# Kernel optimization log

Hardware: AMD Instinct MI355X
Metric: run time of the kernel (lower is better)

## Reference

```python
import jax, jax.numpy as jnp
import numpy as np

B, L, D = 64, 512, 768

def setup_inputs() -> dict:
    key = jax.random.key(0)
    k1, k2, k3, k4 = jax.random.split(key, 4)
    hidden_states = jax.random.normal(k1, (B, L, D), dtype=jnp.float32)
    # nn.Linear(hidden_size, hidden_size): weight [D, D], bias [D]
    W = jax.random.normal(k2, (D, D), dtype=jnp.float32) * (1.0 / np.sqrt(D))
    b = jax.random.normal(k3, (D,), dtype=jnp.float32) * 0.02
    # context_vector: [D, 1]
    context_vector = jax.random.normal(k4, (D, 1), dtype=jnp.float32)
    return {"hidden_states": hidden_states, "W": W, "b": b, "context_vector": context_vector}

def reference(hidden_states, W, b, context_vector):
    # tanh(dense(h)): [B, L, D]; torch Linear uses x @ W.T + b
    proj = jnp.tanh(jnp.einsum('bld,ed->ble', hidden_states, W) + b)
    # scores: [B, L]
    scores = jnp.einsum('bld,d->bl', proj, context_vector[:, 0])
    # softmax over sequence dim (dim=1)
    attention_weights = jax.nn.softmax(scores, axis=1)
    # weighted sum over sequence: [B, D]
    weighted_output = jnp.einsum('bld,bl->bd', hidden_states, attention_weights)
    return (weighted_output, attention_weights)
```

## Files before the change

kernel.cpp:

```cpp
#include <hip/hip_runtime.h>
#include <hip/hip_bf16.h>


using half8 = __attribute__((ext_vector_type(8))) _Float16;
using f32x4 = __attribute__((ext_vector_type(4))) float;

#define AS1 __attribute__((address_space(1)))
#define AS3 __attribute__((address_space(3)))

__device__ __forceinline__ void gload_lds16(const void* g, void* l) {
  __builtin_amdgcn_global_load_lds((const AS1 void*)g, (AS3 void*)l, 16, 0, 0);
}

__device__ __forceinline__ unsigned short f2h(float x) {
  _Float16 h = (_Float16)x;
  return __builtin_bit_cast(unsigned short, h);
}

__device__ __forceinline__ float tanh_fast(float x) {
  return 1.0f - __fdividef(2.0f, 1.0f + __expf(2.0f * x));
}


__global__ void convert_h(const float4* __restrict__ H4, ushort4* __restrict__ Ah) {
  int i = blockIdx.x * 256 + threadIdx.x;
  float4 x = H4[i];
  ushort4 o;
  o.x = f2h(x.x); o.y = f2h(x.y); o.z = f2h(x.z); o.w = f2h(x.w);
  Ah[i] = o;
}

__global__ void convert_w(const float4* __restrict__ W4, ushort4* __restrict__ Wt) {
  int i = blockIdx.x * 256 + threadIdx.x;
  float4 x = W4[i];
  ushort4 o;
  o.x = f2h(x.x); o.y = f2h(x.y); o.z = f2h(x.z); o.w = f2h(x.w);
  Wt[i] = o;
}


__device__ __forceinline__ void stage_tiles32(const char* abase, const char* bbase,
                                              char* ldsAbuf, char* ldsBbuf, int tid) {
  char* ldsAw = ldsAbuf + ((tid >> 6) << 10);
  char* ldsBw = ldsBbuf + ((tid >> 6) << 10);
  #pragma unroll
  for (int r = 0; r < 2; ++r) {
    int off = tid * 16 + r * 4096;
    int row = off >> 6;
    int col = (off & 63) ^ ((row & 3) << 4);
    gload_lds16(abase + row * 1536 + col, ldsAw + r * 4096);
  }
  #pragma unroll
  for (int r = 0; r < 2; ++r) {
    int off = tid * 16 + r * 4096;
    int row = off >> 6;
    int col = (off & 63) ^ ((row & 3) << 4);
    gload_lds16(bbase + row * 1536 + col, ldsBw + r * 4096);
  }
}

__device__ __forceinline__ void compute_tile32(const ushort* ldsAbuf, const ushort* ldsBbuf,
                                               int wr, int wc, int m, int q,
                                               f32x4 acc[4][4]) {
  half8 areg[4], breg[4];
  #pragma unroll
  for (int mi = 0; mi < 4; ++mi) {
    int row = wr * 64 + mi * 16 + m;
    int col = (q * 16) ^ ((row & 3) << 4);
    areg[mi] = *(const half8*)((const char*)ldsAbuf + row * 64 + col);
  }
  #pragma unroll
  for (int ni = 0; ni < 4; ++ni) {
    int row = wc * 64 + ni * 16 + m;
    int col = (q * 16) ^ ((row & 3) << 4);
    breg[ni] = *(const half8*)((const char*)ldsBbuf + row * 64 + col);
  }
  #pragma unroll
  for (int mi = 0; mi < 4; ++mi)
    #pragma unroll
    for (int ni = 0; ni < 4; ++ni)
      acc[mi][ni] = __builtin_amdgcn_mfma_f32_16x16x32_f16(
          areg[mi], breg[ni], acc[mi][ni], 0, 0, 0);
}

__global__ __launch_bounds__(256, 4) void gemm_scores(
    const ushort* __restrict__ Ah, const ushort* __restrict__ Wt,
    const float* __restrict__ bias, const float* __restrict__ cvec,
    float* __restrict__ part) {
  __shared__ ushort ldsA[2][4096];
  __shared__ ushort ldsB[2][4096];
  __shared__ float scpart[2][128];

  const int tid = threadIdx.x;
  const int lane = tid & 63;
  const int wid = tid >> 6;
  const int wr = wid >> 1, wc = wid & 1;
  const int m = lane & 15, q = lane >> 4;

  const int bid = blockIdx.x;
  const int xcd = bid & 7;
  const int slot = bid >> 3;
  const int mtile = xcd * 32 + slot / 6;
  const int ntile = slot % 6;

  f32x4 acc[4][4];
  #pragma unroll
  for (int a = 0; a < 4; ++a)
    #pragma unroll
    for (int b2 = 0; b2 < 4; ++b2)
      acc[a][b2] = (f32x4){0.f, 0.f, 0.f, 0.f};

  const char* const abase0 = (const char*)Ah + (size_t)(mtile * 128) * 1536;
  const char* const bbase0 = (const char*)Wt + (size_t)(ntile * 128) * 1536;

  stage_tiles32(abase0, bbase0, (char*)ldsA[0], (char*)ldsB[0], tid);
  __syncthreads();

  #pragma unroll
  for (int kb2 = 0; kb2 < 12; ++kb2) {
    stage_tiles32(abase0 + (kb2 * 2 + 1) * 64, bbase0 + (kb2 * 2 + 1) * 64,
                  (char*)ldsA[1], (char*)ldsB[1], tid);
    compute_tile32(ldsA[0], ldsB[0], wr, wc, m, q, acc);
    __syncthreads();

    if (kb2 < 11)
      stage_tiles32(abase0 + (kb2 * 2 + 2) * 64, bbase0 + (kb2 * 2 + 2) * 64,
                    (char*)ldsA[0], (char*)ldsB[0], tid);
    compute_tile32(ldsA[1], ldsB[1], wr, wc, m, q, acc);
    __syncthreads();
  }

  float bb[4], cc[4];
  #pragma unroll
  for (int ni = 0; ni < 4; ++ni) {
    int e = ntile * 128 + wc * 64 + ni * 16 + m;
    bb[ni] = bias[e];
    cc[ni] = cvec[e];
  }
  #pragma unroll
  for (int mi = 0; mi < 4; ++mi) {
    #pragma unroll
    for (int j = 0; j < 4; ++j) {
      float s = 0.f;
      #pragma unroll
      for (int ni = 0; ni < 4; ++ni)
        s += tanh_fast(acc[mi][ni][j] + bb[ni]) * cc[ni];
      s += __shfl_xor(s, 1);
      s += __shfl_xor(s, 2);
      s += __shfl_xor(s, 4);
      s += __shfl_xor(s, 8);
      if (m == 0) scpart[wc][wr * 64 + mi * 16 + q * 4 + j] = s;
    }
  }
  __syncthreads();
  if (tid < 128)
    part[ntile * 32768 + mtile * 128 + tid] = scpart[0][tid] + scpart[1][tid];
}

__global__ void wsum_fused(const ushort* __restrict__ Ah, const float* __restrict__ prt,
                           float* __restrict__ out) {
  int b = blockIdx.x, dc = blockIdx.y;
  int t = threadIdx.x;
  __shared__ float w[512];
  __shared__ float redm[2], reds[2];

  float s[4];
  #pragma unroll
  for (int i = 0; i < 4; ++i) {
    int r = b * 512 + t + i * 128;
    s[i] = prt[r] + prt[32768 + r] + prt[2 * 32768 + r] +
           prt[3 * 32768 + r] + prt[4 * 32768 + r] + prt[5 * 32768 + r];
  }
  float mx = fmaxf(fmaxf(s[0], s[1]), fmaxf(s[2], s[3]));
  #pragma unroll
  for (int o = 32; o >= 1; o >>= 1) mx = fmaxf(mx, __shfl_xor(mx, o));
  if ((t & 63) == 0) redm[t >> 6] = mx;
  __syncthreads();
  mx = fmaxf(redm[0], redm[1]);

  float e[4], sm = 0.f;
  #pragma unroll
  for (int i = 0; i < 4; ++i) { e[i] = __expf(s[i] - mx); sm += e[i]; }
  #pragma unroll
  for (int o = 32; o >= 1; o >>= 1) sm += __shfl_xor(sm, o);
  if ((t & 63) == 0) reds[t >> 6] = sm;
  __syncthreads();
  float inv = 1.0f / (reds[0] + reds[1]);
  #pragma unroll
  for (int i = 0; i < 4; ++i) w[t + i * 128] = e[i] * inv;
  __syncthreads();

  int d0 = dc * 256 + t * 2;
  const ushort* hp = Ah + (size_t)b * 512 * 768 + d0;
  float a0 = 0.f, a1 = 0.f;
  #pragma unroll 8
  for (int l = 0; l < 512; ++l) {
    unsigned u = *(const unsigned*)(hp + (size_t)l * 768);
    float wl = w[l];
    a0 += wl * (float)__builtin_bit_cast(_Float16, (unsigned short)(u & 0xffff));
    a1 += wl * (float)__builtin_bit_cast(_Float16, (unsigned short)(u >> 16));
  }
  out[b * 768 + d0] = a0;
  out[b * 768 + d0 + 1] = a1;

  if (dc == 0) {
    #pragma unroll
    for (int i = 0; i < 4; ++i)
      out[49152 + b * 512 + t + i * 128] = w[t + i * 128];
  }
}

extern "C" void kernel_launch(void* const* d_in, const int* in_sizes, int n_in,
                              void* d_out, int out_size, void* d_ws, size_t ws_size,
                              hipStream_t stream) {
  const float* H    = (const float*)d_in[0];
  const float* W    = (const float*)d_in[1];
  const float* bias = (const float*)d_in[2];
  const float* cvec = (const float*)d_in[3];
  float* out = (float*)d_out;

  char* ws = (char*)d_ws;
  ushort* Ah = (ushort*)(ws + 0);
  ushort* Wt = (ushort*)(ws + 50331648);
  float*  prt = (float*)(ws + 51511296);

  hipLaunchKernelGGL(convert_h, dim3(24576), dim3(256), 0, stream,
                     (const float4*)H, (ushort4*)Ah);
  hipLaunchKernelGGL(convert_w, dim3(576), dim3(256), 0, stream,
                     (const float4*)W, (ushort4*)Wt);
  hipLaunchKernelGGL(gemm_scores, dim3(1536), dim3(256), 0, stream,
                     Ah, Wt, bias, cvec, prt);
  hipLaunchKernelGGL(wsum_fused, dim3(64, 3), dim3(128), 0, stream,
                     Ah, prt, out);
}
```

Measured before the change: 117.0 us.

## Restructure score GEMM into 128x256 tiles with 3-stage K=64 pipeline

The score GEMM now uses 512-thread blocks computing 128x256 output tiles, halving the grid and the number of partial-score slices from six to three. It stages K=64 chunks through a triple-buffered LDS pipeline with explicit vmcnt waits, split prefetch issue, and s_setprio around the MFMA bursts. The goal is more reuse of A tiles, fewer barriers per K step, and deeper overlap of global loads with compute. In exchange it uses more LDS per block, so occupancy drops, and the hand-tuned waitcnt logic is fragile.

```diff
diff --git a/kernel.cpp b/kernel.cpp
--- a/kernel.cpp
+++ b/kernel.cpp
@@ -38,102 +38,122 @@
   Wt[i] = o;
 }
 
-
-__device__ __forceinline__ void stage_tiles32(const char* abase, const char* bbase,
-                                              char* ldsAbuf, char* ldsBbuf, int tid) {
-  char* ldsAw = ldsAbuf + ((tid >> 6) << 10);
-  char* ldsBw = ldsBbuf + ((tid >> 6) << 10);
-  #pragma unroll
-  for (int r = 0; r < 2; ++r) {
-    int off = tid * 16 + r * 4096;
-    int row = off >> 6;
-    int col = (off & 63) ^ ((row & 3) << 4);
-    gload_lds16(abase + row * 1536 + col, ldsAw + r * 4096);
-  }
-  #pragma unroll
-  for (int r = 0; r < 2; ++r) {
-    int off = tid * 16 + r * 4096;
-    int row = off >> 6;
-    int col = (off & 63) ^ ((row & 3) << 4);
-    gload_lds16(bbase + row * 1536 + col, ldsBw + r * 4096);
-  }
-}
-
-__device__ __forceinline__ void compute_tile32(const ushort* ldsAbuf, const ushort* ldsBbuf,
-                                               int wr, int wc, int m, int q,
-                                               f32x4 acc[4][4]) {
-  half8 areg[4], breg[4];
-  #pragma unroll
-  for (int mi = 0; mi < 4; ++mi) {
-    int row = wr * 64 + mi * 16 + m;
-    int col = (q * 16) ^ ((row & 3) << 4);
-    areg[mi] = *(const half8*)((const char*)ldsAbuf + row * 64 + col);
-  }
-  #pragma unroll
-  for (int ni = 0; ni < 4; ++ni) {
-    int row = wc * 64 + ni * 16 + m;
-    int col = (q * 16) ^ ((row & 3) << 4);
-    breg[ni] = *(const half8*)((const char*)ldsBbuf + row * 64 + col);
-  }
-  #pragma unroll
-  for (int mi = 0; mi < 4; ++mi)
-    #pragma unroll
-    for (int ni = 0; ni < 4; ++ni)
-      acc[mi][ni] = __builtin_amdgcn_mfma_f32_16x16x32_f16(
-          areg[mi], breg[ni], acc[mi][ni], 0, 0, 0);
-}
-
-__global__ __launch_bounds__(256, 4) void gemm_scores(
+__global__ __launch_bounds__(512) void gemm_scores(
     const ushort* __restrict__ Ah, const ushort* __restrict__ Wt,
     const float* __restrict__ bias, const float* __restrict__ cvec,
     float* __restrict__ part) {
-  __shared__ ushort ldsA[2][4096];
-  __shared__ ushort ldsB[2][4096];
-  __shared__ float scpart[2][128];
+  __shared__ ushort ldsA[3][128 * 64];
+  __shared__ ushort ldsB[3][256 * 64];
+  __shared__ float scpart[4][128];
 
   const int tid = threadIdx.x;
   const int lane = tid & 63;
   const int wid = tid >> 6;
-  const int wr = wid >> 1, wc = wid & 1;
+  const int wr = wid >> 2;
+  const int wc = wid & 3;
   const int m = lane & 15, q = lane >> 4;
 
   const int bid = blockIdx.x;
   const int xcd = bid & 7;
-  const int slot = bid >> 3;
-  const int mtile = xcd * 32 + slot / 6;
-  const int ntile = slot % 6;
+  const int sid = bid >> 3;
+  const int mtile = xcd * 32 + sid / 3;
+  const int ntile = sid % 3;
+
+  const char* const Abase = (const char*)Ah + (size_t)(mtile * 128) * 1536;
+  const char* const Bbase = (const char*)Wt + (size_t)(ntile * 256) * 1536;
+  const int wavebase = (tid >> 6) << 10;
 
   f32x4 acc[4][4];
   #pragma unroll
-  for (int a = 0; a < 4; ++a)
-    #pragma unroll
-    for (int b2 = 0; b2 < 4; ++b2)
-      acc[a][b2] = (f32x4){0.f, 0.f, 0.f, 0.f};
-
-  const char* const abase0 = (const char*)Ah + (size_t)(mtile * 128) * 1536;
-  const char* const bbase0 = (const char*)Wt + (size_t)(ntile * 128) * 1536;
-
-  stage_tiles32(abase0, bbase0, (char*)ldsA[0], (char*)ldsB[0], tid);
-  __syncthreads();
-
-  #pragma unroll
-  for (int kb2 = 0; kb2 < 12; ++kb2) {
-    stage_tiles32(abase0 + (kb2 * 2 + 1) * 64, bbase0 + (kb2 * 2 + 1) * 64,
-                  (char*)ldsA[1], (char*)ldsB[1], tid);
-    compute_tile32(ldsA[0], ldsB[0], wr, wc, m, q, acc);
-    __syncthreads();
-
-    if (kb2 < 11)
-      stage_tiles32(abase0 + (kb2 * 2 + 2) * 64, bbase0 + (kb2 * 2 + 2) * 64,
-                    (char*)ldsA[0], (char*)ldsB[0], tid);
-    compute_tile32(ldsA[1], ldsB[1], wr, wc, m, q, acc);
-    __syncthreads();
+  for (int i = 0; i < 4; ++i)
+    #pragma unroll
+    for (int j = 0; j < 4; ++j)
+      acc[i][j] = (f32x4){0.f, 0.f, 0.f, 0.f};
+
+  auto stageA = [&](int kt, char* dst) {
+    #pragma unroll
+    for (int c = 0; c < 2; ++c) {
+      int off = tid * 16 + c * 8192;
+      int row = off >> 7;
+      int col = (off & 127) ^ ((row & 7) << 4);
+      gload_lds16(Abase + (size_t)row * 1536 + kt * 128 + col,
+                  dst + c * 8192 + wavebase);
+    }
+  };
+  auto stageBq = [&](int kt, char* dst, int c) {
+    int off = tid * 16 + c * 8192;
+    int row = off >> 7;
+    int col = (off & 127) ^ ((row & 7) << 4);
+    gload_lds16(Bbase + (size_t)row * 1536 + kt * 128 + col,
+                dst + c * 8192 + wavebase);
+  };
+
+  stageA(0, (char*)ldsA[0]);
+  #pragma unroll
+  for (int c = 0; c < 4; ++c) stageBq(0, (char*)ldsB[0], c);
+  stageA(1, (char*)ldsA[1]);
+  #pragma unroll
+  for (int c = 0; c < 4; ++c) stageBq(1, (char*)ldsB[1], c);
+  asm volatile("s_waitcnt vmcnt(6)" ::: "memory");
+  __builtin_amdgcn_s_barrier();
+
+  #pragma unroll
+  for (int t = 0; t < 12; ++t) {
+    const char* As = (const char*)ldsA[t % 3];
+    const char* Bs = (const char*)ldsB[t % 3];
+    char* dA = (char*)ldsA[(t + 2) % 3];
+    char* dB = (char*)ldsB[(t + 2) % 3];
+    const int st = t + 2;
+    half8 breg[4][2];
+    #pragma unroll
+    for (int p = 0; p < 2; ++p) {
+      half8 areg[2][2];
+      #pragma unroll
+      for (int dmi = 0; dmi < 2; ++dmi) {
+        int row = wr * 64 + (p * 2 + dmi) * 16 + m;
+        #pragma unroll
+        for (int ks = 0; ks < 2; ++ks)
+          areg[dmi][ks] = *(const half8*)(As + row * 128 +
+                                          ((ks * 64 + q * 16) ^ ((m & 7) << 4)));
+      }
+      if (p == 0) {
+        #pragma unroll
+        for (int ni = 0; ni < 4; ++ni) {
+          int row = wc * 64 + ni * 16 + m;
+          #pragma unroll
+          for (int ks = 0; ks < 2; ++ks)
+            breg[ni][ks] = *(const half8*)(Bs + row * 128 +
+                                           ((ks * 64 + q * 16) ^ ((m & 7) << 4)));
+        }
+      }
+      if (st < 12) {
+        if (p == 0) { stageA(st, dA); stageBq(st, dB, 0); }
+        else        { stageBq(st, dB, 1); stageBq(st, dB, 2); stageBq(st, dB, 3); }
+      }
+      if (p == 1) {
+        if (t < 10)       asm volatile("s_waitcnt vmcnt(6)" ::: "memory");
+        else if (t == 10) asm volatile("s_waitcnt vmcnt(0)" ::: "memory");
+      }
+      __builtin_amdgcn_s_barrier();
+      asm volatile("s_waitcnt lgkmcnt(0)" ::: "memory");
+      __builtin_amdgcn_s_setprio(1);
+      #pragma unroll
+      for (int ks = 0; ks < 2; ++ks)
+        #pragma unroll
+        for (int dmi = 0; dmi < 2; ++dmi)
+          #pragma unroll
+          for (int ni = 0; ni < 4; ++ni)
+            acc[p * 2 + dmi][ni] = __builtin_amdgcn_mfma_f32_16x16x32_f16(
+                areg[dmi][ks], breg[ni][ks], acc[p * 2 + dmi][ni], 0, 0, 0);
+      __builtin_amdgcn_s_setprio(0);
+      __builtin_amdgcn_s_barrier();
+    }
   }
 
   float bb[4], cc[4];
   #pragma unroll
   for (int ni = 0; ni < 4; ++ni) {
-    int e = ntile * 128 + wc * 64 + ni * 16 + m;
+    int e = ntile * 256 + wc * 64 + ni * 16 + m;
     bb[ni] = bias[e];
     cc[ni] = cvec[e];
   }
@@ -154,7 +174,8 @@
   }
   __syncthreads();
   if (tid < 128)
-    part[ntile * 32768 + mtile * 128 + tid] = scpart[0][tid] + scpart[1][tid];
+    part[ntile * 32768 + mtile * 128 + tid] =
+        scpart[0][tid] + scpart[1][tid] + scpart[2][tid] + scpart[3][tid];
 }
 
 __global__ void wsum_fused(const ushort* __restrict__ Ah, const float* __restrict__ prt,
@@ -168,8 +189,7 @@
   #pragma unroll
   for (int i = 0; i < 4; ++i) {
     int r = b * 512 + t + i * 128;
-    s[i] = prt[r] + prt[32768 + r] + prt[2 * 32768 + r] +
-           prt[3 * 32768 + r] + prt[4 * 32768 + r] + prt[5 * 32768 + r];
+    s[i] = prt[r] + prt[32768 + r] + prt[2 * 32768 + r];
   }
   float mx = fmaxf(fmaxf(s[0], s[1]), fmaxf(s[2], s[3]));
   #pragma unroll
@@ -228,7 +248,7 @@
                      (const float4*)H, (ushort4*)Ah);
   hipLaunchKernelGGL(convert_w, dim3(576), dim3(256), 0, stream,
                      (const float4*)W, (ushort4*)Wt);
-  hipLaunchKernelGGL(gemm_scores, dim3(1536), dim3(256), 0, stream,
+  hipLaunchKernelGGL(gemm_scores, dim3(768), dim3(512), 0, stream,
                      Ah, Wt, bias, cvec, prt);
   hipLaunchKernelGGL(wsum_fused, dim3(64, 3), dim3(128), 0, stream,
                      Ah, prt, out);
```

Measured after the change: 111.9 us. 1.05x faster.

## Compute full N=768 per block in GEMM, removing partial score reduction

Applied to the files above, without the earlier changes.

The GEMM now gives each 512-thread block a 128-row M tile across all 768 output columns, with 8 waves each covering 64x192. This removes the six-way N split, the partial-score buffer, and the six-way sum in the softmax kernel, and each A tile is loaded only once. In exchange the block holds 192 accumulator floats per thread and about 100KB of LDS, and the grid shrinks to 256 blocks. That lowers occupancy and may underfill the GPU's 256 CUs if spills or load imbalance occur.

```diff
diff --git a/kernel.cpp b/kernel.cpp
--- a/kernel.cpp
+++ b/kernel.cpp
@@ -38,102 +38,81 @@
   Wt[i] = o;
 }
 
-
-__device__ __forceinline__ void stage_tiles32(const char* abase, const char* bbase,
-                                              char* ldsAbuf, char* ldsBbuf, int tid) {
-  char* ldsAw = ldsAbuf + ((tid >> 6) << 10);
-  char* ldsBw = ldsBbuf + ((tid >> 6) << 10);
-  #pragma unroll
-  for (int r = 0; r < 2; ++r) {
-    int off = tid * 16 + r * 4096;
-    int row = off >> 6;
-    int col = (off & 63) ^ ((row & 3) << 4);
-    gload_lds16(abase + row * 1536 + col, ldsAw + r * 4096);
-  }
-  #pragma unroll
-  for (int r = 0; r < 2; ++r) {
-    int off = tid * 16 + r * 4096;
-    int row = off >> 6;
-    int col = (off & 63) ^ ((row & 3) << 4);
-    gload_lds16(bbase + row * 1536 + col, ldsBw + r * 4096);
-  }
-}
-
-__device__ __forceinline__ void compute_tile32(const ushort* ldsAbuf, const ushort* ldsBbuf,
-                                               int wr, int wc, int m, int q,
-                                               f32x4 acc[4][4]) {
-  half8 areg[4], breg[4];
-  #pragma unroll
-  for (int mi = 0; mi < 4; ++mi) {
-    int row = wr * 64 + mi * 16 + m;
-    int col = (q * 16) ^ ((row & 3) << 4);
-    areg[mi] = *(const half8*)((const char*)ldsAbuf + row * 64 + col);
-  }
-  #pragma unroll
-  for (int ni = 0; ni < 4; ++ni) {
-    int row = wc * 64 + ni * 16 + m;
-    int col = (q * 16) ^ ((row & 3) << 4);
-    breg[ni] = *(const half8*)((const char*)ldsBbuf + row * 64 + col);
-  }
-  #pragma unroll
-  for (int mi = 0; mi < 4; ++mi)
-    #pragma unroll
-    for (int ni = 0; ni < 4; ++ni)
-      acc[mi][ni] = __builtin_amdgcn_mfma_f32_16x16x32_f16(
-          areg[mi], breg[ni], acc[mi][ni], 0, 0, 0);
-}
-
-__global__ __launch_bounds__(256, 4) void gemm_scores(
+__global__ __launch_bounds__(512) void gemm_scores(
     const ushort* __restrict__ Ah, const ushort* __restrict__ Wt,
     const float* __restrict__ bias, const float* __restrict__ cvec,
     float* __restrict__ part) {
   __shared__ ushort ldsA[2][4096];
-  __shared__ ushort ldsB[2][4096];
-  __shared__ float scpart[2][128];
+  __shared__ ushort ldsB[2][24576];
+  __shared__ float scpart[4][128];
 
   const int tid = threadIdx.x;
   const int lane = tid & 63;
   const int wid = tid >> 6;
-  const int wr = wid >> 1, wc = wid & 1;
+  const int wr = wid >> 2;
+  const int wc = wid & 3;
   const int m = lane & 15, q = lane >> 4;
-
-  const int bid = blockIdx.x;
-  const int xcd = bid & 7;
-  const int slot = bid >> 3;
-  const int mtile = xcd * 32 + slot / 6;
-  const int ntile = slot % 6;
-
-  f32x4 acc[4][4];
-  #pragma unroll
-  for (int a = 0; a < 4; ++a)
-    #pragma unroll
-    for (int b2 = 0; b2 < 4; ++b2)
-      acc[a][b2] = (f32x4){0.f, 0.f, 0.f, 0.f};
-
-  const char* const abase0 = (const char*)Ah + (size_t)(mtile * 128) * 1536;
-  const char* const bbase0 = (const char*)Wt + (size_t)(ntile * 128) * 1536;
-
-  stage_tiles32(abase0, bbase0, (char*)ldsA[0], (char*)ldsB[0], tid);
-  __syncthreads();
-
-  #pragma unroll
-  for (int kb2 = 0; kb2 < 12; ++kb2) {
-    stage_tiles32(abase0 + (kb2 * 2 + 1) * 64, bbase0 + (kb2 * 2 + 1) * 64,
-                  (char*)ldsA[1], (char*)ldsB[1], tid);
-    compute_tile32(ldsA[0], ldsB[0], wr, wc, m, q, acc);
+  const int mtile = blockIdx.x;
+
+  const char* const Abase = (const char*)Ah + (size_t)(mtile * 128) * 1536;
+  const char* const Bbase = (const char*)Wt;
+
+  const int alr = tid >> 3;
+  const int au = (tid & 7) ^ (alr & 7);
+  const size_t asrc = (size_t)(alr + 64 * (au >> 2)) * 1536 + (au & 3) * 16;
+  const int bu = (tid & 7) ^ ((tid >> 3) & 7);
+  const size_t bsrc0 = (size_t)((tid >> 3) + 384 * (bu >> 2)) * 1536 + (bu & 3) * 16;
+  const int wavebase = wid << 10;
+
+  f32x4 acc[4][12];
+  #pragma unroll
+  for (int i = 0; i < 4; ++i)
+    #pragma unroll
+    for (int j = 0; j < 12; ++j)
+      acc[i][j] = (f32x4){0.f, 0.f, 0.f, 0.f};
+
+  auto stage = [&](int kt, int s) {
+    gload_lds16(Abase + asrc + kt * 64, (char*)ldsA[s] + wavebase);
+    #pragma unroll
+    for (int c = 0; c < 6; ++c)
+      gload_lds16(Bbase + bsrc0 + c * 98304 + kt * 64,
+                  (char*)ldsB[s] + c * 8192 + wavebase);
+  };
+
+  const int aslot = ((wr * 4 + q) ^ (m & 7)) * 16;
+  const int bslot = (((wc >> 1) * 4 + q) ^ (m & 7)) * 16;
+  const int blr0 = (wc & 1) * 192;
+
+  auto compute = [&](int s) {
+    const char* Ab = (const char*)ldsA[s];
+    const char* Bb = (const char*)ldsB[s];
+    half8 areg[4];
+    #pragma unroll
+    for (int mi = 0; mi < 4; ++mi)
+      areg[mi] = *(const half8*)(Ab + (mi * 16 + m) * 128 + aslot);
+    #pragma unroll
+    for (int ni = 0; ni < 12; ++ni) {
+      half8 breg = *(const half8*)(Bb + (blr0 + ni * 16 + m) * 128 + bslot);
+      #pragma unroll
+      for (int mi = 0; mi < 4; ++mi)
+        acc[mi][ni] = __builtin_amdgcn_mfma_f32_16x16x32_f16(
+            areg[mi], breg, acc[mi][ni], 0, 0, 0);
+    }
+  };
+
+  stage(0, 0);
+  __syncthreads();
+  #pragma unroll 2
+  for (int t = 0; t < 24; ++t) {
+    if (t + 1 < 24) stage(t + 1, (t + 1) & 1);
+    compute(t & 1);
     __syncthreads();
-
-    if (kb2 < 11)
-      stage_tiles32(abase0 + (kb2 * 2 + 2) * 64, bbase0 + (kb2 * 2 + 2) * 64,
-                    (char*)ldsA[0], (char*)ldsB[0], tid);
-    compute_tile32(ldsA[1], ldsB[1], wr, wc, m, q, acc);
-    __syncthreads();
-  }
-
-  float bb[4], cc[4];
-  #pragma unroll
-  for (int ni = 0; ni < 4; ++ni) {
-    int e = ntile * 128 + wc * 64 + ni * 16 + m;
+  }
+
+  float bb[12], cc[12];
+  #pragma unroll
+  for (int ni = 0; ni < 12; ++ni) {
+    int e = wc * 192 + ni * 16 + m;
     bb[ni] = bias[e];
     cc[ni] = cvec[e];
   }
@@ -143,7 +122,7 @@
     for (int j = 0; j < 4; ++j) {
       float s = 0.f;
       #pragma unroll
-      for (int ni = 0; ni < 4; ++ni)
+      for (int ni = 0; ni < 12; ++ni)
         s += tanh_fast(acc[mi][ni][j] + bb[ni]) * cc[ni];
       s += __shfl_xor(s, 1);
       s += __shfl_xor(s, 2);
@@ -154,7 +133,8 @@
   }
   __syncthreads();
   if (tid < 128)
-    part[ntile * 32768 + mtile * 128 + tid] = scpart[0][tid] + scpart[1][tid];
+    part[mtile * 128 + tid] =
+        scpart[0][tid] + scpart[1][tid] + scpart[2][tid] + scpart[3][tid];
 }
 
 __global__ void wsum_fused(const ushort* __restrict__ Ah, const float* __restrict__ prt,
@@ -166,11 +146,7 @@
 
   float s[4];
   #pragma unroll
-  for (int i = 0; i < 4; ++i) {
-    int r = b * 512 + t + i * 128;
-    s[i] = prt[r] + prt[32768 + r] + prt[2 * 32768 + r] +
-           prt[3 * 32768 + r] + prt[4 * 32768 + r] + prt[5 * 32768 + r];
-  }
+  for (int i = 0; i < 4; ++i) s[i] = prt[b * 512 + t + i * 128];
   float mx = fmaxf(fmaxf(s[0], s[1]), fmaxf(s[2], s[3]));
   #pragma unroll
   for (int o = 32; o >= 1; o >>= 1) mx = fmaxf(mx, __shfl_xor(mx, o));
@@ -228,7 +204,7 @@
                      (const float4*)H, (ushort4*)Ah);
   hipLaunchKernelGGL(convert_w, dim3(576), dim3(256), 0, stream,
                      (const float4*)W, (ushort4*)Wt);
-  hipLaunchKernelGGL(gemm_scores, dim3(1536), dim3(256), 0, stream,
+  hipLaunchKernelGGL(gemm_scores, dim3(256), dim3(512), 0, stream,
                      Ah, Wt, bias, cvec, prt);
   hipLaunchKernelGGL(wsum_fused, dim3(64, 3), dim3(128), 0, stream,
                      Ah, prt, out);
```

Result: no change. 114.9 us (-1.8%).
